# Performance work log

Measured on AMD Instinct MI355X. Metric: run time of the kernel, lower is better.

The kernel has to match this reference:

```python
import jax, jax.numpy as jnp
import numpy as np

H_DIM = 768
N_HEADS = 12
HEAD_DIM = H_DIM // N_HEADS  # 64
LOW_RANK = 2
LR_DIM = H_DIM // LOW_RANK   # 384
SEQ = 2048
WINDOW = 1024
EOT = 50256


def _rope_tables(seq_len, dim):
    pos = jnp.arange(seq_len, dtype=jnp.float32)[:, None]
    div = jnp.exp(jnp.arange(0, dim, 2, dtype=jnp.float32) * (-np.log(10000.0) / dim))
    emb = pos * div  # (S, dim/2)
    sin = jnp.concatenate([jnp.sin(emb), jnp.sin(emb)], axis=-1)  # (S, dim)
    cos = jnp.concatenate([jnp.cos(emb), jnp.cos(emb)], axis=-1)
    return sin, cos


def _apply_rope(x, sin, cos):
    # x: (B, H, S, d); sin/cos: (S, d)
    half = x.shape[-1] // 2
    rot = jnp.concatenate([-x[..., half:], x[..., :half]], axis=-1)
    return x * cos + rot * sin


def setup_inputs() -> dict:
    key = jax.random.key(0)
    ks = jax.random.split(key, 20)
    x = jax.random.normal(ks[0], (1, SEQ, H_DIM), dtype=jnp.float32)
    # tokens with document boundaries every ~512 tokens
    tok = jax.random.randint(ks[1], (SEQ,), 0, 50257)
    tok = tok.at[::512].set(EOT)

    def lin(k, fan_in, fan_out):
        w = jax.random.normal(k, (fan_in, fan_out), dtype=jnp.float32) * 0.02
        b = jnp.zeros((fan_out,), dtype=jnp.float32)
        return w, b

    qd_w, qd_b = lin(ks[2], H_DIM, LR_DIM)
    qu_w, qu_b = lin(ks[3], LR_DIM, H_DIM)
    qr_w, qr_b = lin(ks[4], H_DIM, HEAD_DIM)
    kvd_w, kvd_b = lin(ks[5], H_DIM, LR_DIM)
    ku_w, ku_b = lin(ks[6], LR_DIM, H_DIM)
    vu_w, vu_b = lin(ks[7], LR_DIM, H_DIM * 2)
    kr_w, kr_b = lin(ks[8], H_DIM, HEAD_DIM)
    o_w, o_b = lin(ks[9], H_DIM * 2, H_DIM)
    return dict(x=x, token_seq=tok,
                qd_w=qd_w, qd_b=qd_b, qu_w=qu_w, qu_b=qu_b,
                qr_w=qr_w, qr_b=qr_b, kvd_w=kvd_w, kvd_b=kvd_b,
                ku_w=ku_w, ku_b=ku_b, vu_w=vu_w, vu_b=vu_b,
                kr_w=kr_w, kr_b=kr_b, o_w=o_w, o_b=o_b)


def _mla_forward(x, token_seq, qd_w, qd_b, qu_w, qu_b, qr_w, qr_b,
                 kvd_w, kvd_b, ku_w, ku_b, vu_w, vu_b, kr_w, kr_b, o_w, o_b):
    B, S, _ = x.shape
    sin, cos = _rope_tables(S, HEAD_DIM)
    scale = (2 * HEAD_DIM) ** (-0.5)

    # queries: low-rank down/up + shared rotary part
    q = (x @ qd_w + qd_b) @ qu_w + qu_b                     # (B,S,H_DIM)
    q = q.reshape(B, S, N_HEADS, HEAD_DIM).transpose(0, 2, 1, 3)
    qr = (x @ qr_w + qr_b)[:, None, :, :]                   # (B,1,S,hd)
    qr = jnp.broadcast_to(qr, (B, N_HEADS, S, HEAD_DIM))
    qr = _apply_rope(qr, sin, cos)
    q = jnp.concatenate([q, qr], axis=-1)                   # (B,nh,S,2hd)

    # shared low-rank kv latent
    lkv = x @ kvd_w + kvd_b                                 # (B,S,LR)
    k = (lkv @ ku_w + ku_b).reshape(B, S, N_HEADS, HEAD_DIM).transpose(0, 2, 1, 3)
    kr = (x @ kr_w + kr_b)[:, None, :, :]
    kr = jnp.broadcast_to(kr, (B, N_HEADS, S, HEAD_DIM))
    kr = _apply_rope(kr, sin, cos)
    k = jnp.concatenate([k, kr], axis=-1)                   # (B,nh,S,2hd)

    v = (lkv @ vu_w + vu_b).reshape(B, S, N_HEADS, 2 * HEAD_DIM).transpose(0, 2, 1, 3)

    # mask: causal & same-document & sliding window (<1024)
    docs = jnp.cumsum(token_seq == EOT)
    qi = jnp.arange(S)
    mask = (qi[:, None] >= qi[None, :]) \
           & (docs[:, None] == docs[None, :]) \
           & (qi[:, None] - qi[None, :] < WINDOW)           # (S,S)

    scores = jnp.einsum('bhqd,bhkd->bhqk', q, k) * scale
    scores = jnp.where(mask, scores, -jnp.inf)
    attn = jax.nn.softmax(scores, axis=-1)
    out = jnp.einsum('bhqk,bhkd->bhqd', attn, v)            # (B,nh,S,2hd)
    out = out.transpose(0, 2, 1, 3).reshape(B, S, 2 * H_DIM)
    return out @ o_w + o_b


def reference(x, token_seq, qd_w, qd_b, qu_w, qu_b, qr_w, qr_b,
              kvd_w, kvd_b, ku_w, ku_b, vu_w, vu_b, kr_w, kr_b, o_w, o_b):
    return _mla_forward(x, token_seq, qd_w, qd_b, qu_w, qu_b, qr_w, qr_b,
                        kvd_w, kvd_b, ku_w, ku_b, vu_w, vu_b, kr_w, kr_b, o_w, o_b)
```

## Files before the change

kernel.cpp:

```cpp
#include <hip/hip_runtime.h>
#include <hip/hip_bf16.h>
#include <math.h>

#define SEQ 2048
#define HDIM 768
#define NH 12
#define HD 64
#define LR 384
#define EOT 50256

typedef short s16x8 __attribute__((ext_vector_type(8)));
typedef float f32x4 __attribute__((ext_vector_type(4)));
typedef unsigned short u16x8 __attribute__((ext_vector_type(8)));
typedef unsigned short u16x4 __attribute__((ext_vector_type(4)));

__device__ __forceinline__ unsigned short f2bf(float f) {
    union { float f; unsigned u; } v; v.f = f;
    unsigned r = v.u + 0x7fffu + ((v.u >> 16) & 1u);
    return (unsigned short)(r >> 16);
}

__device__ __forceinline__ void gl_lds16(const void* g, void* l) {
    __builtin_amdgcn_global_load_lds(
        (const __attribute__((address_space(1))) unsigned int*)g,
        (__attribute__((address_space(3))) unsigned int*)l, 16, 0, 0);
}

__global__ __launch_bounds__(256)
void transpose_pack_all(const float* w0, const float* w1, const float* w2, const float* w3,
                        const float* w4, const float* w5, const float* w6, const float* w7,
                        unsigned short* t0, unsigned short* t1, unsigned short* t2, unsigned short* t3,
                        unsigned short* t4, unsigned short* t5, unsigned short* t6, unsigned short* t7,
                        const float* x, unsigned short* xb,
                        const float* qd_b, const float* kvd_b, const float* qr_b, const float* kr_b,
                        const float* qu_b, const float* ku_b, const float* vu_b,
                        float* biasA, float* biasB,
                        const int* tok, int* lastEOT) {
    __shared__ float t[64][65];
    __shared__ int smax[256];
    int b = blockIdx.x;
    const int tid = threadIdx.x;
    if (b == 1129) {
        const int base = tid * 8;
        int v[8];
        int mx = 0;
#pragma unroll
        for (int j = 0; j < 8; ++j) {
            int i = base + j;
            int f = (tok[i] == EOT) ? i : 0;
            mx = max(mx, f);
            v[j] = mx;
        }
        smax[tid] = mx;
        __syncthreads();
        for (int off = 1; off < 256; off <<= 1) {
            int val = (tid >= off) ? smax[tid - off] : 0;
            __syncthreads();
            smax[tid] = max(smax[tid], val);
            __syncthreads();
        }
        int pre = (tid > 0) ? smax[tid - 1] : 0;
#pragma unroll
        for (int j = 0; j < 8; ++j) lastEOT[base + j] = max(pre, v[j]);
        return;
    }
    if (b == 1128) {
        for (int i = tid; i < 896; i += 256) {
            float v;
            if (i < 384) v = qd_b[i];
            else if (i < 768) v = kvd_b[i - 384];
            else if (i < 832) v = qr_b[i - 768];
            else v = kr_b[i - 832];
            biasA[i] = v;
        }
        for (int i = tid; i < 3072; i += 256) {
            float v;
            if (i < 768) v = qu_b[i];
            else if (i < 1536) v = ku_b[i - 768];
            else v = vu_b[i - 1536];
            biasB[i] = v;
        }
        return;
    }
    if (b >= 744) {
        int b2 = b - 744;
        int row0 = (b2 / 12) * 64, col0 = (b2 % 12) * 64;
#pragma unroll
        for (int i = 0; i < 16; ++i) {
            int idx = tid + i * 256;
            int r = idx >> 6, c = idx & 63;
            xb[(size_t)(row0 + r) * HDIM + col0 + c] = f2bf(x[(size_t)(row0 + r) * HDIM + col0 + c]);
        }
        return;
    }
    const float* W; unsigned short* T; int K, N, lt;
    if      (b < 72)  { W = w0; T = t0; K = 768;  N = 384;  lt = b; }
    else if (b < 144) { W = w1; T = t1; K = 384;  N = 768;  lt = b - 72; }
    else if (b < 156) { W = w2; T = t2; K = 768;  N = 64;   lt = b - 144; }
    else if (b < 228) { W = w3; T = t3; K = 768;  N = 384;  lt = b - 156; }
    else if (b < 300) { W = w4; T = t4; K = 384;  N = 768;  lt = b - 228; }
    else if (b < 444) { W = w5; T = t5; K = 384;  N = 1536; lt = b - 300; }
    else if (b < 456) { W = w6; T = t6; K = 768;  N = 64;   lt = b - 444; }
    else              { W = w7; T = t7; K = 1536; N = 768;  lt = b - 456; }
    const int tn = N >> 6;
    const int n0 = (lt % tn) * 64, k0 = (lt / tn) * 64;
#pragma unroll
    for (int i = 0; i < 16; ++i) {
        int idx = tid + i * 256;
        int k = idx >> 6, n = idx & 63;
        t[k][n] = W[(size_t)(k0 + k) * N + n0 + n];
    }
    __syncthreads();
#pragma unroll
    for (int i = 0; i < 16; ++i) {
        int idx = tid + i * 256;
        int n = idx >> 6, k = idx & 63;
        T[(size_t)(n0 + n) * K + k0 + k] = f2bf(t[k][n]);
    }
}

template <int FUSE, int BM, int BN>
__global__ __launch_bounds__(256)
void gemm_mfma_kernel(const unsigned short* __restrict__ A, const unsigned short* __restrict__ Bt,
                      const float* __restrict__ bias,
                      void* __restrict__ O0, void* __restrict__ O1, void* __restrict__ O2,
                      int K, int lda) {
    constexpr int MI = BM / 32;
    constexpr int NI = BN / 32;
    constexpr int AI = BM / 32;
    constexpr int BI = BN / 32;
    __shared__ unsigned short As[2][BM * 64];
    __shared__ unsigned short Bs[2][BN * 64];
    const int tid = threadIdx.x;
    const int w = tid >> 6, lane = tid & 63, lr = lane & 15, lg = lane >> 4;
    const int row0 = blockIdx.y * BM, col0 = blockIdx.x * BN;
    const int wr = (w >> 1) * (BM / 2), wc = (w & 1) * (BN / 2);
    const unsigned short* Ab = A + ((FUSE == 2 && col0 >= 768) ? 384 : 0);

    f32x4 acc[MI][NI];
#pragma unroll
    for (int i = 0; i < MI; ++i)
#pragma unroll
        for (int j = 0; j < NI; ++j) acc[i][j] = f32x4{0.f, 0.f, 0.f, 0.f};

    auto stage = [&](int buf, int kt) {
#pragma unroll
        for (int i = 0; i < AI; ++i) {
            int c = tid + i * 256;
            int row = c >> 3, dgL = c & 7;
            gl_lds16(Ab + (size_t)(row0 + row) * lda + kt + (dgL ^ (row & 7)) * 8, &As[buf][c * 8]);
        }
#pragma unroll
        for (int i = 0; i < BI; ++i) {
            int c = tid + i * 256;
            int n = c >> 3, dgL = c & 7;
            gl_lds16(Bt + (size_t)(col0 + n) * K + kt + (dgL ^ (n & 7)) * 8, &Bs[buf][c * 8]);
        }
    };

    const int nkt = K >> 6;
    stage(0, 0);
    for (int t = 0; t < nkt; ++t) {
        __syncthreads();
        if (t + 1 < nkt) stage((t + 1) & 1, (t + 1) << 6);
        const unsigned short* asb = As[t & 1];
        const unsigned short* bsb = Bs[t & 1];
#pragma unroll
        for (int kk = 0; kk < 2; ++kk) {
            const int kbyte = kk * 64 + lg * 16;
#pragma unroll
            for (int mi = 0; mi < MI; ++mi) {
                const int row = wr + mi * 16 + lr;
                s16x8 a = *(const s16x8*)&asb[row * 64 + ((kbyte ^ ((row & 7) << 4)) >> 1)];
#pragma unroll
                for (int ni = 0; ni < NI; ++ni) {
                    const int n = wc + ni * 16 + lr;
                    s16x8 bfr = *(const s16x8*)&bsb[n * 64 + ((kbyte ^ ((n & 7) << 4)) >> 1)];
                    acc[mi][ni] = __builtin_amdgcn_mfma_f32_16x16x32_bf16(a, bfr, acc[mi][ni], 0, 0, 0);
                }
            }
        }
    }

    if constexpr (FUSE == 1) {
        if (col0 >= 768) {
            __syncthreads();
            float* rt = (float*)&As[0][0];
#pragma unroll
            for (int mi = 0; mi < MI; ++mi)
#pragma unroll
                for (int ni = 0; ni < NI; ++ni) {
                    const int cl = wc + ni * 16 + lr;
                    const float bv = bias[col0 + cl];
#pragma unroll
                    for (int j = 0; j < 4; ++j)
                        rt[(wr + mi * 16 + lg * 4 + j) * 64 + cl] = acc[mi][ni][j] + bv;
                }
            __syncthreads();
            unsigned short* dst = (col0 == 768) ? (unsigned short*)O1 : (unsigned short*)O2;
            constexpr int TPR = 256 / BM;
            constexpr int CNT = 32 / TPR;
            const int row = tid / TPR;
            const int i0 = (tid % TPR) * CNT;
            const float srow = (float)(row0 + row);
#pragma unroll
            for (int ii = 0; ii < CNT; ++ii) {
                const int i = i0 + ii;
                float a = rt[row * 64 + i], b = rt[row * 64 + 32 + i];
                float div = expf((float)(2 * i) * (-logf(10000.0f) / 64.0f));
                float emb = srow * div;
                float sn, cs;
                __sincosf(emb, &sn, &cs);
                dst[(size_t)(row0 + row) * 64 + i]      = f2bf(a * cs - b * sn);
                dst[(size_t)(row0 + row) * 64 + 32 + i] = f2bf(b * cs + a * sn);
            }
            return;
        }
    }

#pragma unroll
    for (int mi = 0; mi < MI; ++mi) {
#pragma unroll
        for (int ni = 0; ni < NI; ++ni) {
            const int col = col0 + wc + ni * 16 + lr;
            const float bv = bias[col];
            const int rbase = row0 + wr + mi * 16 + lg * 4;
            if (FUSE == 0) {
#pragma unroll
                for (int j = 0; j < 4; ++j)
                    ((float*)O0)[(size_t)(rbase + j) * HDIM + col] = acc[mi][ni][j] + bv;
            } else if (FUSE == 1) {
#pragma unroll
                for (int j = 0; j < 4; ++j)
                    ((unsigned short*)O0)[(size_t)(rbase + j) * HDIM + col] = f2bf(acc[mi][ni][j] + bv);
            } else {
                if (col < 768) {
                    const int hh = col >> 6, d = col & 63;
#pragma unroll
                    for (int j = 0; j < 4; ++j)
                        ((unsigned short*)O0)[(size_t)(rbase + j) * (NH * 64) + hh * 64 + d] = f2bf(acc[mi][ni][j] + bv);
                } else if (col < 1536) {
                    const int c2 = col - 768;
                    const int hh = c2 >> 6, d = c2 & 63;
#pragma unroll
                    for (int j = 0; j < 4; ++j)
                        ((unsigned short*)O1)[(size_t)(rbase + j) * (NH * 64) + hh * 64 + d] = f2bf(acc[mi][ni][j] + bv);
                } else {
                    const int c2 = col - 1536;
                    const int hh = c2 >> 7, d = c2 & 127;
                    u16x4 pk;
#pragma unroll
                    for (int j = 0; j < 4; ++j) pk[j] = f2bf(acc[mi][ni][j] + bv);
                    *(u16x4*)((unsigned short*)O2 + (size_t)(hh * 128 + d) * SEQ + rbase) = pk;
                }
            }
        }
    }
}

__global__ __launch_bounds__(256)
void attn_mfma_kernel(const unsigned short* __restrict__ qbuf,
                      const unsigned short* __restrict__ qrb,
                      const unsigned short* __restrict__ kbuf,
                      const unsigned short* __restrict__ krb,
                      const unsigned short* __restrict__ vbT,
                      const int* __restrict__ lastEOT,
                      unsigned short* __restrict__ aob) {
    __shared__ unsigned short Ks[2][64 * 128];
    __shared__ unsigned short Vt[2][128 * 64];
    __shared__ unsigned short Pa[4][16 * 64];

    const int h    = blockIdx.y;
    const int q0   = blockIdx.x * 64;
    const int tid  = threadIdx.x;
    const int w    = tid >> 6;
    const int lane = tid & 63;
    const int lr   = lane & 15;
    const int lg   = lane >> 4;

    const int qrow0 = q0 + w * 16 + lg * 4;
    const int qminw = q0 + w * 16;
    const int qmaxw = qminw + 15;
    const int leMinW = lastEOT[qminw];
    const int leMaxW = lastEOT[qmaxw];
    int rs[4];
#pragma unroll
    for (int r = 0; r < 4; ++r) rs[r] = lastEOT[qrow0 + r];

    s16x8 aq[4];
    {
        const int s = q0 + w * 16 + lr;
        const unsigned short* qp = qbuf + ((size_t)s * NH + h) * 64 + lg * 8;
        aq[0] = *(const s16x8*)qp;
        aq[1] = *(const s16x8*)(qp + 32);
        const unsigned short* qrp = qrb + (size_t)s * 64 + lg * 8;
        aq[2] = *(const s16x8*)qrp;
        aq[3] = *(const s16x8*)(qrp + 32);
    }

    const int kt0 = lastEOT[q0] & ~63;
    const int ntiles = (q0 + 64 - kt0) >> 6;

    float lsum[4] = {0.f, 0.f, 0.f, 0.f};
    f32x4 o[8];
#pragma unroll
    for (int n = 0; n < 8; ++n) o[n] = f32x4{0.f, 0.f, 0.f, 0.f};

    const float scl2 = 0.088388347648318447f * 1.4426950408889634f;

    auto stage = [&](int buf, int k0) {
#pragma unroll
        for (int i = 0; i < 4; ++i) {
            const int c = tid + i * 256;
            const int key = c >> 4, dgL = c & 15;
            const int dg = dgL ^ (key & 7);
            const unsigned short* src = (dg < 8)
                ? kbuf + ((size_t)(k0 + key) * NH + h) * 64 + dg * 8
                : krb + (size_t)(k0 + key) * 64 + (dg - 8) * 8;
            gl_lds16(src, &Ks[buf][c * 8]);
        }
#pragma unroll
        for (int i = 0; i < 4; ++i) {
            const int c = tid + i * 256;
            const int dim = c >> 3, kgL = c & 7;
            gl_lds16(vbT + ((size_t)h * 128 + dim) * SEQ + k0 + (kgL ^ (dim & 7)) * 8, &Vt[buf][c * 8]);
        }
    };

    stage(0, kt0);
    for (int t = 0; t < ntiles; ++t) {
        const int k0 = kt0 + t * 64;
        __syncthreads();
        if (t + 1 < ntiles) stage((t + 1) & 1, k0 + 64);

        if (k0 > qmaxw || k0 + 63 < leMinW) continue;

        const unsigned short* ksb = Ks[t & 1];
        const unsigned short* vtb = Vt[t & 1];

        f32x4 s[4];
#pragma unroll
        for (int n = 0; n < 4; ++n) s[n] = f32x4{0.f, 0.f, 0.f, 0.f};
#pragma unroll
        for (int n = 0; n < 4; ++n) {
            const int key = n * 16 + lr;
            const int swz = (key & 7) << 4;
#pragma unroll
            for (int kk = 0; kk < 4; ++kk) {
                const int colb = (kk * 64 + lg * 16) ^ swz;
                s16x8 bk = *(const s16x8*)&ksb[key * 128 + (colb >> 1)];
                s[n] = __builtin_amdgcn_mfma_f32_16x16x32_bf16(aq[kk], bk, s[n], 0, 0, 0);
            }
        }

        const bool full = (k0 + 63 <= qminw) && (k0 >= leMaxW);
        float p[4][4];
        if (full) {
#pragma unroll
            for (int n = 0; n < 4; ++n)
#pragma unroll
                for (int r = 0; r < 4; ++r) {
                    float pv = exp2f(s[n][r] * scl2);
                    p[n][r] = pv;
                    lsum[r] += pv;
                }
        } else {
#pragma unroll
            for (int n = 0; n < 4; ++n) {
                const int k = k0 + n * 16 + lr;
#pragma unroll
                for (int r = 0; r < 4; ++r) {
                    const int qq = qrow0 + r;
                    const bool valid = (k <= qq) && (k >= rs[r]);
                    float pv = valid ? exp2f(s[n][r] * scl2) : 0.f;
                    p[n][r] = pv;
                    lsum[r] += pv;
                }
            }
        }

#pragma unroll
        for (int n = 0; n < 4; ++n)
#pragma unroll
            for (int r = 0; r < 4; ++r) {
                const int ql = lg * 4 + r;
                const int key = n * 16 + lr;
                const int byteoff = (key * 2) ^ ((ql & 7) << 4);
                Pa[w][ql * 64 + (byteoff >> 1)] = f2bf(p[n][r]);
            }

#pragma unroll
        for (int kk2 = 0; kk2 < 2; ++kk2) {
            const int keyb = kk2 * 32 + lg * 8;
            s16x8 ap = *(const s16x8*)&Pa[w][lr * 64 + ((((keyb * 2) ^ ((lr & 7) << 4))) >> 1)];
#pragma unroll
            for (int n = 0; n < 8; ++n) {
                const int dim = n * 16 + lr;
                s16x8 bv = *(const s16x8*)&vtb[dim * 64 + ((((keyb * 2) ^ ((dim & 7) << 4))) >> 1)];
                o[n] = __builtin_amdgcn_mfma_f32_16x16x32_bf16(ap, bv, o[n], 0, 0, 0);
            }
        }
    }

#pragma unroll
    for (int off = 1; off < 16; off <<= 1)
#pragma unroll
        for (int r = 0; r < 4; ++r) lsum[r] += __shfl_xor(lsum[r], off);

    float inv[4];
#pragma unroll
    for (int r = 0; r < 4; ++r) inv[r] = 1.f / lsum[r];
#pragma unroll
    for (int n = 0; n < 8; ++n)
#pragma unroll
        for (int r = 0; r < 4; ++r) {
            const int qq = qrow0 + r;
            aob[(size_t)qq * (2 * HDIM) + h * 128 + n * 16 + lr] = f2bf(o[n][r] * inv[r]);
        }
}

extern "C" void kernel_launch(void* const* d_in, const int* in_sizes, int n_in,
                              void* d_out, int out_size, void* d_ws, size_t ws_size,
                              hipStream_t stream) {
    (void)in_sizes; (void)n_in; (void)out_size; (void)ws_size;
    const float* x     = (const float*)d_in[0];
    const int*   tok   = (const int*)d_in[1];
    const float* qd_w  = (const float*)d_in[2];
    const float* qd_b  = (const float*)d_in[3];
    const float* qu_w  = (const float*)d_in[4];
    const float* qu_b  = (const float*)d_in[5];
    const float* qr_w  = (const float*)d_in[6];
    const float* qr_b  = (const float*)d_in[7];
    const float* kvd_w = (const float*)d_in[8];
    const float* kvd_b = (const float*)d_in[9];
    const float* ku_w  = (const float*)d_in[10];
    const float* ku_b  = (const float*)d_in[11];
    const float* vu_w  = (const float*)d_in[12];
    const float* vu_b  = (const float*)d_in[13];
    const float* kr_w  = (const float*)d_in[14];
    const float* kr_b  = (const float*)d_in[15];
    const float* o_w   = (const float*)d_in[16];
    const float* o_b   = (const float*)d_in[17];
    float* out = (float*)d_out;

    unsigned short* ws = (unsigned short*)d_ws;
    unsigned short* xb   = ws;
    unsigned short* lqkv = xb   + (size_t)SEQ * HDIM;
    unsigned short* qbuf = lqkv + (size_t)SEQ * HDIM;
    unsigned short* kbuf = qbuf + (size_t)SEQ * NH * 64;
    unsigned short* qrb  = kbuf + (size_t)SEQ * NH * 64;
    unsigned short* krb  = qrb  + (size_t)SEQ * 64;
    unsigned short* vbT  = krb  + (size_t)SEQ * 64;
    unsigned short* aob  = vbT  + (size_t)NH * 128 * SEQ;
    unsigned short* B1   = aob  + (size_t)SEQ * 2 * HDIM;
    unsigned short* B2   = B1   + (size_t)896 * HDIM;
    unsigned short* to   = B2   + (size_t)3072 * LR;
    float* biasA = (float*)(to + (size_t)HDIM * 2 * HDIM);
    float* biasB = biasA + 896;
    int* lastEOT = (int*)(biasB + 3072);

    unsigned short* tqd  = B1;
    unsigned short* tkvd = B1 + (size_t)384 * 768;
    unsigned short* tqr  = B1 + (size_t)768 * 768;
    unsigned short* tkr  = B1 + (size_t)832 * 768;
    unsigned short* tqu  = B2;
    unsigned short* tku  = B2 + (size_t)768 * 384;
    unsigned short* tvu  = B2 + (size_t)1536 * 384;

    transpose_pack_all<<<1130, 256, 0, stream>>>(qd_w, qu_w, qr_w, kvd_w, ku_w, vu_w, kr_w, o_w,
                                                 tqd, tqu, tqr, tkvd, tku, tvu, tkr, to,
                                                 x, xb, qd_b, kvd_b, qr_b, kr_b, qu_b, ku_b, vu_b,
                                                 biasA, biasB, tok, lastEOT);

    gemm_mfma_kernel<1, 64, 64><<<dim3(14, 32), 256, 0, stream>>>(xb, B1, biasA, lqkv, qrb, krb, HDIM, HDIM);
    gemm_mfma_kernel<2, 128, 128><<<dim3(24, 16), 256, 0, stream>>>(lqkv, B2, biasB, qbuf, kbuf, vbT, LR, HDIM);

    attn_mfma_kernel<<<dim3(SEQ / 64, NH), 256, 0, stream>>>(qbuf, qrb, kbuf, krb, vbT, lastEOT, aob);

    gemm_mfma_kernel<0, 64, 64><<<dim3(12, 32), 256, 0, stream>>>(aob, to, o_b, out, nullptr, nullptr, 2 * HDIM, 2 * HDIM);
}
```

Before: 78.29 us.

## Vectorize pack loads, single-buffer attention staging, narrow second GEMM tile

The transpose/pack kernel now reads float4 and writes 4-wide bf16 vectors instead of scalars, cutting memory instruction count. The attention kernel drops double-buffered K/V shared memory in favour of a single buffer with a second barrier per tile. LDS use roughly halves, which may allow more resident blocks, but loads no longer overlap compute. The up-projection GEMM switches from 128x128 to 128x64 tiles, doubling the grid for better CU coverage.

```diff
diff --git a/kernel.cpp b/kernel.cpp
--- a/kernel.cpp
+++ b/kernel.cpp
@@ -86,10 +86,12 @@
         int b2 = b - 744;
         int row0 = (b2 / 12) * 64, col0 = (b2 % 12) * 64;
 #pragma unroll
-        for (int i = 0; i < 16; ++i) {
+        for (int i = 0; i < 4; ++i) {
             int idx = tid + i * 256;
-            int r = idx >> 6, c = idx & 63;
-            xb[(size_t)(row0 + r) * HDIM + col0 + c] = f2bf(x[(size_t)(row0 + r) * HDIM + col0 + c]);
+            int r = idx >> 4, c4 = (idx & 15) * 4;
+            float4 v = *(const float4*)(x + (size_t)(row0 + r) * HDIM + col0 + c4);
+            u16x4 pk = {f2bf(v.x), f2bf(v.y), f2bf(v.z), f2bf(v.w)};
+            *(u16x4*)(xb + (size_t)(row0 + r) * HDIM + col0 + c4) = pk;
         }
         return;
     }
@@ -105,17 +107,19 @@
     const int tn = N >> 6;
     const int n0 = (lt % tn) * 64, k0 = (lt / tn) * 64;
 #pragma unroll
-    for (int i = 0; i < 16; ++i) {
+    for (int i = 0; i < 4; ++i) {
         int idx = tid + i * 256;
-        int k = idx >> 6, n = idx & 63;
-        t[k][n] = W[(size_t)(k0 + k) * N + n0 + n];
+        int k = idx >> 4, c4 = (idx & 15) * 4;
+        float4 v = *(const float4*)(W + (size_t)(k0 + k) * N + n0 + c4);
+        t[k][c4] = v.x; t[k][c4 + 1] = v.y; t[k][c4 + 2] = v.z; t[k][c4 + 3] = v.w;
     }
     __syncthreads();
 #pragma unroll
-    for (int i = 0; i < 16; ++i) {
+    for (int i = 0; i < 4; ++i) {
         int idx = tid + i * 256;
-        int n = idx >> 6, k = idx & 63;
-        T[(size_t)(n0 + n) * K + k0 + k] = f2bf(t[k][n]);
+        int n = idx >> 4, k4 = (idx & 15) * 4;
+        u16x4 pk = {f2bf(t[k4][n]), f2bf(t[k4 + 1][n]), f2bf(t[k4 + 2][n]), f2bf(t[k4 + 3][n])};
+        *(u16x4*)(T + (size_t)(n0 + n) * K + k0 + k4) = pk;
     }
 }
 
@@ -266,8 +270,8 @@
                       const unsigned short* __restrict__ vbT,
                       const int* __restrict__ lastEOT,
                       unsigned short* __restrict__ aob) {
-    __shared__ unsigned short Ks[2][64 * 128];
-    __shared__ unsigned short Vt[2][128 * 64];
+    __shared__ unsigned short Ks[64 * 128];
+    __shared__ unsigned short Vt[128 * 64];
     __shared__ unsigned short Pa[4][16 * 64];
 
     const int h    = blockIdx.y;
@@ -308,7 +312,7 @@
 
     const float scl2 = 0.088388347648318447f * 1.4426950408889634f;
 
-    auto stage = [&](int buf, int k0) {
+    auto stage = [&](int k0) {
 #pragma unroll
         for (int i = 0; i < 4; ++i) {
             const int c = tid + i * 256;
@@ -317,89 +321,89 @@
             const unsigned short* src = (dg < 8)
                 ? kbuf + ((size_t)(k0 + key) * NH + h) * 64 + dg * 8
                 : krb + (size_t)(k0 + key) * 64 + (dg - 8) * 8;
-            gl_lds16(src, &Ks[buf][c * 8]);
+            gl_lds16(src, &Ks[c * 8]);
         }
 #pragma unroll
         for (int i = 0; i < 4; ++i) {
             const int c = tid + i * 256;
             const int dim = c >> 3, kgL = c & 7;
-            gl_lds16(vbT + ((size_t)h * 128 + dim) * SEQ + k0 + (kgL ^ (dim & 7)) * 8, &Vt[buf][c * 8]);
+            gl_lds16(vbT + ((size_t)h * 128 + dim) * SEQ + k0 + (kgL ^ (dim & 7)) * 8, &Vt[c * 8]);
         }
     };
 
-    stage(0, kt0);
+    stage(kt0);
     for (int t = 0; t < ntiles; ++t) {
         const int k0 = kt0 + t * 64;
         __syncthreads();
-        if (t + 1 < ntiles) stage((t + 1) & 1, k0 + 64);
-
-        if (k0 > qmaxw || k0 + 63 < leMinW) continue;
-
-        const unsigned short* ksb = Ks[t & 1];
-        const unsigned short* vtb = Vt[t & 1];
-
-        f32x4 s[4];
-#pragma unroll
-        for (int n = 0; n < 4; ++n) s[n] = f32x4{0.f, 0.f, 0.f, 0.f};
-#pragma unroll
-        for (int n = 0; n < 4; ++n) {
-            const int key = n * 16 + lr;
-            const int swz = (key & 7) << 4;
-#pragma unroll
-            for (int kk = 0; kk < 4; ++kk) {
-                const int colb = (kk * 64 + lg * 16) ^ swz;
-                s16x8 bk = *(const s16x8*)&ksb[key * 128 + (colb >> 1)];
-                s[n] = __builtin_amdgcn_mfma_f32_16x16x32_bf16(aq[kk], bk, s[n], 0, 0, 0);
-            }
-        }
-
-        const bool full = (k0 + 63 <= qminw) && (k0 >= leMaxW);
-        float p[4][4];
-        if (full) {
+
+        const bool skip = (k0 > qmaxw || k0 + 63 < leMinW);
+        if (!skip) {
+            f32x4 s[4];
+#pragma unroll
+            for (int n = 0; n < 4; ++n) s[n] = f32x4{0.f, 0.f, 0.f, 0.f};
+#pragma unroll
+            for (int n = 0; n < 4; ++n) {
+                const int key = n * 16 + lr;
+                const int swz = (key & 7) << 4;
+#pragma unroll
+                for (int kk = 0; kk < 4; ++kk) {
+                    const int colb = (kk * 64 + lg * 16) ^ swz;
+                    s16x8 bk = *(const s16x8*)&Ks[key * 128 + (colb >> 1)];
+                    s[n] = __builtin_amdgcn_mfma_f32_16x16x32_bf16(aq[kk], bk, s[n], 0, 0, 0);
+                }
+            }
+
+            const bool full = (k0 + 63 <= qminw) && (k0 >= leMaxW);
+            float p[4][4];
+            if (full) {
+#pragma unroll
+                for (int n = 0; n < 4; ++n)
+#pragma unroll
+                    for (int r = 0; r < 4; ++r) {
+                        float pv = exp2f(s[n][r] * scl2);
+                        p[n][r] = pv;
+                        lsum[r] += pv;
+                    }
+            } else {
+#pragma unroll
+                for (int n = 0; n < 4; ++n) {
+                    const int k = k0 + n * 16 + lr;
+#pragma unroll
+                    for (int r = 0; r < 4; ++r) {
+                        const int qq = qrow0 + r;
+                        const bool valid = (k <= qq) && (k >= rs[r]);
+                        float pv = valid ? exp2f(s[n][r] * scl2) : 0.f;
+                        p[n][r] = pv;
+                        lsum[r] += pv;
+                    }
+                }
+            }
+
 #pragma unroll
             for (int n = 0; n < 4; ++n)
 #pragma unroll
                 for (int r = 0; r < 4; ++r) {
-                    float pv = exp2f(s[n][r] * scl2);
-                    p[n][r] = pv;
-                    lsum[r] += pv;
-                }
-        } else {
-#pragma unroll
-            for (int n = 0; n < 4; ++n) {
-                const int k = k0 + n * 16 + lr;
-#pragma unroll
-                for (int r = 0; r < 4; ++r) {
-                    const int qq = qrow0 + r;
-                    const bool valid = (k <= qq) && (k >= rs[r]);
-                    float pv = valid ? exp2f(s[n][r] * scl2) : 0.f;
-                    p[n][r] = pv;
-                    lsum[r] += pv;
-                }
-            }
-        }
-
-#pragma unroll
-        for (int n = 0; n < 4; ++n)
-#pragma unroll
-            for (int r = 0; r < 4; ++r) {
-                const int ql = lg * 4 + r;
-                const int key = n * 16 + lr;
-                const int byteoff = (key * 2) ^ ((ql & 7) << 4);
-                Pa[w][ql * 64 + (byteoff >> 1)] = f2bf(p[n][r]);
-            }
-
-#pragma unroll
-        for (int kk2 = 0; kk2 < 2; ++kk2) {
-            const int keyb = kk2 * 32 + lg * 8;
-            s16x8 ap = *(const s16x8*)&Pa[w][lr * 64 + ((((keyb * 2) ^ ((lr & 7) << 4))) >> 1)];
-#pragma unroll
-            for (int n = 0; n < 8; ++n) {
-                const int dim = n * 16 + lr;
-                s16x8 bv = *(const s16x8*)&vtb[dim * 64 + ((((keyb * 2) ^ ((dim & 7) << 4))) >> 1)];
-                o[n] = __builtin_amdgcn_mfma_f32_16x16x32_bf16(ap, bv, o[n], 0, 0, 0);
-            }
-        }
+                    const int ql = lg * 4 + r;
+                    const int key = n * 16 + lr;
+                    const int byteoff = (key * 2) ^ ((ql & 7) << 4);
+                    Pa[w][ql * 64 + (byteoff >> 1)] = f2bf(p[n][r]);
+                }
+
+#pragma unroll
+            for (int kk2 = 0; kk2 < 2; ++kk2) {
+                const int keyb = kk2 * 32 + lg * 8;
+                s16x8 ap = *(const s16x8*)&Pa[w][lr * 64 + ((((keyb * 2) ^ ((lr & 7) << 4))) >> 1)];
+#pragma unroll
+                for (int n = 0; n < 8; ++n) {
+                    const int dim = n * 16 + lr;
+                    s16x8 bv = *(const s16x8*)&Vt[dim * 64 + ((((keyb * 2) ^ ((dim & 7) << 4))) >> 1)];
+                    o[n] = __builtin_amdgcn_mfma_f32_16x16x32_bf16(ap, bv, o[n], 0, 0, 0);
+                }
+            }
+        }
+
+        __syncthreads();
+        if (t + 1 < ntiles) stage(k0 + 64);
     }
 
 #pragma unroll
@@ -473,7 +477,7 @@
                                                  biasA, biasB, tok, lastEOT);
 
     gemm_mfma_kernel<1, 64, 64><<<dim3(14, 32), 256, 0, stream>>>(xb, B1, biasA, lqkv, qrb, krb, HDIM, HDIM);
-    gemm_mfma_kernel<2, 128, 128><<<dim3(24, 16), 256, 0, stream>>>(lqkv, B2, biasB, qbuf, kbuf, vbT, LR, HDIM);
+    gemm_mfma_kernel<2, 128, 64><<<dim3(48, 16), 256, 0, stream>>>(lqkv, B2, biasB, qbuf, kbuf, vbT, LR, HDIM);
 
     attn_mfma_kernel<<<dim3(SEQ / 64, NH), 256, 0, stream>>>(qbuf, qrb, kbuf, krb, vbT, lastEOT, aob);
 
```

Result: faster. 74.97 us, median of 3 (-4.2%).
